# Kernel optimization log

Measured on AMD Instinct MI355X. Metric: run time of the kernel, lower is better.

The kernel has to match this reference:

```python
import math
import jax, jax.numpy as jnp
import numpy as np

EMBED, HEADS, LEVELS, POINTS = 256, 8, 4, 4
HEAD_DIM = EMBED // HEADS
SHAPES = ((100, 100), (50, 50), (25, 25), (13, 13))  # (h, w) per level
BS, NQ = 8, 900
NV = sum(h * w for h, w in SHAPES)


def _offset_bias():
    # Faithful to init_weights(): per-head rotated grid init for sampling_offsets bias.
    th = np.arange(HEADS, dtype=np.float32) * (2.0 * math.pi / HEADS)
    g = np.stack([np.cos(th), np.sin(th)], -1)
    g = g / np.abs(g).max(-1, keepdims=True)
    g = np.tile(g[:, None, None, :], (1, LEVELS, POINTS, 1))
    g = g * (np.arange(POINTS, dtype=np.float32) + 1.0)[None, None, :, None]
    return jnp.asarray(g.reshape(-1))


def setup_inputs() -> dict:
    key = jax.random.key(0)
    ks = jax.random.split(key, 10)
    s = 0.05
    return {
        "query": jax.random.normal(ks[0], (BS, NQ, EMBED), jnp.float32),
        "value": jax.random.normal(ks[1], (BS, NV, EMBED), jnp.float32),
        "reference_points": jax.random.uniform(ks[2], (BS, NQ, LEVELS, 2), jnp.float32),
        "spatial_shapes": jnp.array(SHAPES, jnp.int32),
        "W_off": jax.random.normal(ks[3], (EMBED, HEADS * LEVELS * POINTS * 2), jnp.float32) * s,
        "b_off": _offset_bias(),
        "W_attn": jax.random.normal(ks[4], (EMBED, HEADS * LEVELS * POINTS), jnp.float32) * s,
        "b_attn": jnp.zeros((HEADS * LEVELS * POINTS,), jnp.float32),
        "W_v": jax.random.normal(ks[5], (EMBED, EMBED), jnp.float32) * s,
        "b_v": jnp.zeros((EMBED,), jnp.float32),
        "W_out": jax.random.normal(ks[6], (EMBED, EMBED), jnp.float32) * s,
        "b_out": jnp.zeros((EMBED,), jnp.float32),
    }


def _bilinear_sample(vl, loc, H, W, aw):
    """grid_sample bilinear, align_corners=False, zero padding, fused with attn weights.

    vl:  (bs, heads, H*W, d)   loc: (bs, nq, heads, P, 2) in [0,1] (x, y)
    aw:  (bs, heads, nq, P)    ->   (bs, heads, nq, d)
    """
    x = loc[..., 0] * W - 0.5
    y = loc[..., 1] * H - 0.5
    x0 = jnp.floor(x)
    y0 = jnp.floor(y)
    lx = x - x0
    ly = y - y0
    x0i = x0.astype(jnp.int32)
    y0i = y0.astype(jnp.int32)
    bs, heads = vl.shape[0], vl.shape[1]
    nq, P = loc.shape[1], loc.shape[3]
    acc = jnp.zeros((bs, heads, nq, vl.shape[-1]), vl.dtype)
    corners = ((0, 0, (1 - lx) * (1 - ly)), (1, 0, lx * (1 - ly)),
               (0, 1, (1 - lx) * ly), (1, 1, lx * ly))
    for dx, dy, wgt in corners:
        xi = x0i + dx
        yi = y0i + dy
        valid = ((xi >= 0) & (xi < W) & (yi >= 0) & (yi < H)).astype(vl.dtype)
        idx = jnp.clip(yi, 0, H - 1) * W + jnp.clip(xi, 0, W - 1)  # (bs, nq, heads, P)
        idx = idx.transpose(0, 2, 1, 3).reshape(bs, heads, nq * P)
        g = jnp.take_along_axis(vl, idx[..., None], axis=2).reshape(bs, heads, nq, P, -1)
        cw = (wgt * valid).transpose(0, 2, 1, 3) * aw  # (bs, heads, nq, P)
        acc = acc + (g * cw[..., None]).sum(3)
    return acc


def reference(query, value, reference_points, spatial_shapes,
              W_off, b_off, W_attn, b_attn, W_v, b_v, W_out, b_out):
    identity = query
    bs, nq, _ = query.shape
    v = (value @ W_v + b_v).reshape(bs, -1, HEADS, HEAD_DIM)
    off = (query @ W_off + b_off).reshape(bs, nq, HEADS, LEVELS, POINTS, 2)
    aw = (query @ W_attn + b_attn).reshape(bs, nq, HEADS, LEVELS * POINTS)
    aw = jax.nn.softmax(aw, -1).reshape(bs, nq, HEADS, LEVELS, POINTS)
    # offset normalizer is (w, h) per level
    norm = jnp.stack([spatial_shapes[:, 1], spatial_shapes[:, 0]], -1).astype(query.dtype)
    loc = reference_points[:, :, None, :, None, :] + off / norm[None, None, None, :, None, :]
    sizes = [h * w for h, w in SHAPES]
    starts = np.cumsum([0] + sizes[:-1])
    out = jnp.zeros((bs, HEADS, nq, HEAD_DIM), query.dtype)
    for l, (h, w) in enumerate(SHAPES):
        vl = jax.lax.dynamic_slice_in_dim(v, int(starts[l]), sizes[l], axis=1)
        vl = vl.transpose(0, 2, 1, 3)  # (bs, heads, h*w, d)
        aw_l = aw[:, :, :, l].transpose(0, 2, 1, 3)  # (bs, heads, nq, P)
        out = out + _bilinear_sample(vl, loc[:, :, :, l], h, w, aw_l)
    out = out.transpose(0, 2, 1, 3).reshape(bs, nq, EMBED)
    return out @ W_out + b_out + identity
```

## Files before the change

kernel.cpp:

```cpp
#include <hip/hip_runtime.h>
#include <hip/hip_bf16.h>

#define EMBED    256
#define HEADS    8
#define LEVELS   4
#define POINTS   4
#define HEAD_DIM 32
#define BS       8
#define NQ       900
#define NV       13294
#define MV       (BS*NV)
#define MQ       (BS*NQ)
#define NQOUT    384

typedef float  f32x4  __attribute__((ext_vector_type(4)));
typedef __bf16 bf16x8 __attribute__((ext_vector_type(8)));
typedef unsigned short ushort8  __attribute__((ext_vector_type(8)));
typedef unsigned short ushort4v __attribute__((ext_vector_type(4)));

__device__ __forceinline__ unsigned short f2bf(float f) {
    unsigned u = __builtin_bit_cast(unsigned, f);
    u += 0x7FFFu + ((u >> 16) & 1u);
    return (unsigned short)(u >> 16);
}
__device__ __forceinline__ float bf2f(unsigned short h) {
    unsigned u = ((unsigned)h) << 16;
    return __builtin_bit_cast(float, u);
}

__global__ __launch_bounds__(256) void prep_kernel(
    const float* __restrict__ Wv,  const float* __restrict__ Woff,
    const float* __restrict__ Wattn, const float* __restrict__ Wout,
    const float* __restrict__ boff, const float* __restrict__ battn,
    unsigned short* __restrict__ WtV, unsigned short* __restrict__ WtQ,
    unsigned short* __restrict__ WtO, float* __restrict__ biasQ)
{
    int n = blockIdx.x;
    int k = threadIdx.x;
    if (n < 256) {
        WtV[n * 256 + k] = f2bf(Wv [k * 256 + n]);
        WtO[n * 256 + k] = f2bf(Wout[k * 256 + n]);
        WtQ[n * 256 + k] = f2bf(Woff[k * 256 + n]);
    } else {
        int j = n - 256;
        WtQ[n * 256 + k] = f2bf(Wattn[k * 128 + j]);
    }
    if (k == 0) biasQ[n] = (n < 256) ? boff[n] : battn[n - 256];
}

#define WLDK 264

template <int COLSETS, int PAR, bool OUT_BF16, bool ADD_ID>
__global__ __launch_bounds__(COLSETS * PAR * 64)
void gemm_ldsw(const float* __restrict__ A,
               const unsigned short* __restrict__ Bt,
               const float* __restrict__ bias,
               const float* __restrict__ Ident,
               void* __restrict__ Cv, int M, int Ntot)
{
    constexpr int NC   = COLSETS * 64;
    constexpr int NTHR = COLSETS * PAR * 64;
    const int n0g = blockIdx.y * NC;
    __shared__ unsigned short Ws[NC * WLDK];

    const int tid = threadIdx.x;
    #pragma unroll
    for (int i = 0; i < (NC * 32) / NTHR; ++i) {
        int flat = i * NTHR + tid;
        int row = flat >> 5, col = (flat & 31) * 8;
        *(ushort8*)&Ws[row * WLDK + col] =
            *(const ushort8*)(Bt + (size_t)(n0g + row) * 256 + col);
    }
    __syncthreads();

    const int wave = tid >> 6, lane = tid & 63;
    const int colset = wave % COLSETS, parity = wave / COLSETS;
    const int lrow = lane & 15, kq = lane >> 4;
    const int n0 = colset * 64;

    f32x4 bj[4];
    #pragma unroll
    for (int j = 0; j < 4; ++j)
        bj[j] = *(const f32x4*)(bias + n0g + n0 + j * 16 + kq * 4);

    const int NS    = M / 16;
    const int chunk = (NS + gridDim.x - 1) / gridDim.x;
    const int send  = min(NS, blockIdx.x * chunk + chunk);
    int s = blockIdx.x * chunk + parity;
    if (s >= send) return;

    auto loadHalf = [&](f32x4 (&b)[8], int ss, int h) {
        const float* ab = A + (size_t)(ss * 16 + lrow) * 256 + h * 128 + kq * 8;
        #pragma unroll
        for (int c = 0; c < 4; ++c) {
            b[2 * c]     = *(const f32x4*)(ab + c * 32);
            b[2 * c + 1] = *(const f32x4*)(ab + c * 32 + 4);
        }
    };
    auto computeHalf = [&](f32x4 (&b)[8], int h, f32x4 (&acc)[4]) {
        #pragma unroll
        for (int c = 0; c < 4; ++c) {
            ushort8 vb;
            #pragma unroll
            for (int e = 0; e < 4; ++e) {
                vb[e]     = f2bf(b[2 * c][e]);
                vb[4 + e] = f2bf(b[2 * c + 1][e]);
            }
            bf16x8 vf = __builtin_bit_cast(bf16x8, vb);
            #pragma unroll
            for (int j = 0; j < 4; ++j) {
                bf16x8 wf = *(const bf16x8*)
                    &Ws[(n0 + j * 16 + lrow) * WLDK + h * 128 + c * 32 + kq * 8];
                acc[j] = __builtin_amdgcn_mfma_f32_16x16x32_bf16(wf, vf, acc[j], 0, 0, 0);
            }
        }
    };

    f32x4 b0[8], b1[8];
    loadHalf(b0, s, 0);
    while (true) {
        loadHalf(b1, s, 1);
        f32x4 acc[4];
        #pragma unroll
        for (int j = 0; j < 4; ++j) acc[j] = (f32x4)0.f;
        computeHalf(b0, 0, acc);
        const int sn = s + PAR;
        const bool more = sn < send;
        if (more) loadHalf(b0, sn, 0);
        computeHalf(b1, 1, acc);

        const size_t crow = (size_t)(s * 16 + lrow) * Ntot + n0g + n0 + kq * 4;
        #pragma unroll
        for (int j = 0; j < 4; ++j) {
            f32x4 r = acc[j] + bj[j];
            if (ADD_ID)
                r += *(const f32x4*)(Ident + crow + j * 16);
            if (OUT_BF16) {
                ushort4v o;
                #pragma unroll
                for (int e = 0; e < 4; ++e) o[e] = f2bf(r[e]);
                *(ushort4v*)((unsigned short*)Cv + crow + j * 16) = o;
            } else {
                *(f32x4*)((float*)Cv + crow + j * 16) = r;
            }
        }
        if (!more) break;
        s = sn;
    }
}

__device__ const int   LVL_W[4]  = {100, 50, 25, 13};
__device__ const int   LVL_H[4]  = {100, 50, 25, 13};
__device__ const int   LVL_S[4]  = {0, 10000, 12500, 13125};

__global__ __launch_bounds__(256) void sample_kernel(
    const unsigned short* __restrict__ V,
    const float* __restrict__ Qout,
    const float* __restrict__ RP,
    float* __restrict__ OutS)
{
    const int gid = blockIdx.x * 16 + (threadIdx.x >> 4);
    const int s   = threadIdx.x & 15;
    const int h   = gid & 7;
    const int bq  = gid >> 3;
    const int b   = bq / NQ;

    const float* qrow = Qout + (size_t)bq * NQOUT;

    const int l = s >> 2;
    const float ox = qrow[h * 32 + 2 * s];
    const float oy = qrow[h * 32 + 2 * s + 1];
    float logit    = qrow[256 + h * 16 + s];
    const float rpx = RP[((size_t)bq * 4 + l) * 2 + 0];
    const float rpy = RP[((size_t)bq * 4 + l) * 2 + 1];
    const int W = LVL_W[l], H = LVL_H[l], st = LVL_S[l];
    float x = rpx * (float)W + ox - 0.5f;
    float y = rpy * (float)H + oy - 0.5f;
    float fx = floorf(x), fy = floorf(y);
    float lx = x - fx, ly = y - fy;
    int x0 = (int)fx, y0 = (int)fy;
    int x1 = x0 + 1,  y1 = y0 + 1;

    float mx = logit;
    #pragma unroll
    for (int o = 8; o; o >>= 1) mx = fmaxf(mx, __shfl_xor(mx, o, 16));
    float e = __expf(logit - mx);
    float sum = e;
    #pragma unroll
    for (int o = 8; o; o >>= 1) sum += __shfl_xor(sum, o, 16);
    const float wgt = e / sum;

    const float vx0 = (x0 >= 0 && x0 < W) ? 1.f : 0.f;
    const float vx1 = (x1 >= 0 && x1 < W) ? 1.f : 0.f;
    const float vy0 = (y0 >= 0 && y0 < H) ? 1.f : 0.f;
    const float vy1 = (y1 >= 0 && y1 < H) ? 1.f : 0.f;
    const int cx0 = min(max(x0, 0), W - 1), cx1 = min(max(x1, 0), W - 1);
    const int cy0 = min(max(y0, 0), H - 1), cy1 = min(max(y1, 0), H - 1);
    float w00 = wgt * (1.f - lx) * (1.f - ly) * vx0 * vy0;
    float w10 = wgt * lx * (1.f - ly) * vx1 * vy0;
    float w01 = wgt * (1.f - lx) * ly * vx0 * vy1;
    float w11 = wgt * lx * ly * vx1 * vy1;
    int i00 = st + cy0 * W + cx0;
    int i10 = st + cy0 * W + cx1;
    int i01 = st + cy1 * W + cx0;
    int i11 = st + cy1 * W + cx1;

    const unsigned short* vb = V + ((size_t)b * NV) * 256 + h * 32 + 2 * s;
    float ax0 = 0.f, ay0 = 0.f, ax1 = 0.f, ay1 = 0.f;

    #pragma unroll
    for (int sp = 0; sp < 16; ++sp) {
        int   j00 = __shfl(i00, sp, 16), j10 = __shfl(i10, sp, 16);
        int   j01 = __shfl(i01, sp, 16), j11 = __shfl(i11, sp, 16);
        float u00 = __shfl(w00, sp, 16), u10 = __shfl(w10, sp, 16);
        float u01 = __shfl(w01, sp, 16), u11 = __shfl(w11, sp, 16);
        unsigned p00 = *(const unsigned*)(vb + (size_t)j00 * 256);
        unsigned p10 = *(const unsigned*)(vb + (size_t)j10 * 256);
        unsigned p01 = *(const unsigned*)(vb + (size_t)j01 * 256);
        unsigned p11 = *(const unsigned*)(vb + (size_t)j11 * 256);
        ax0 = fmaf(u00, bf2f((unsigned short)(p00 & 0xFFFF)), ax0);
        ay0 = fmaf(u00, bf2f((unsigned short)(p00 >> 16)), ay0);
        ax1 = fmaf(u10, bf2f((unsigned short)(p10 & 0xFFFF)), ax1);
        ay1 = fmaf(u10, bf2f((unsigned short)(p10 >> 16)), ay1);
        ax0 = fmaf(u01, bf2f((unsigned short)(p01 & 0xFFFF)), ax0);
        ay0 = fmaf(u01, bf2f((unsigned short)(p01 >> 16)), ay0);
        ax1 = fmaf(u11, bf2f((unsigned short)(p11 & 0xFFFF)), ax1);
        ay1 = fmaf(u11, bf2f((unsigned short)(p11 >> 16)), ay1);
    }
    float2* o = (float2*)(OutS + (size_t)bq * 256 + h * 32);
    o[s] = make_float2(ax0 + ax1, ay0 + ay1);
}

extern "C" void kernel_launch(void* const* d_in, const int* in_sizes, int n_in,
                              void* d_out, int out_size, void* d_ws, size_t ws_size,
                              hipStream_t stream)
{
    const float* query  = (const float*)d_in[0];
    const float* value  = (const float*)d_in[1];
    const float* rp     = (const float*)d_in[2];
    const float* W_off  = (const float*)d_in[4];
    const float* b_off  = (const float*)d_in[5];
    const float* W_attn = (const float*)d_in[6];
    const float* b_attn = (const float*)d_in[7];
    const float* W_v    = (const float*)d_in[8];
    const float* b_v    = (const float*)d_in[9];
    const float* W_out  = (const float*)d_in[10];
    const float* b_out  = (const float*)d_in[11];

    char* ws = (char*)d_ws;
    size_t off = 0;
    unsigned short* Vbf = (unsigned short*)(ws + off); off += (size_t)MV * 256 * 2;
    float* qout         = (float*)(ws + off);          off += (size_t)MQ * NQOUT * 4;
    float* outs         = (float*)(ws + off);          off += (size_t)MQ * 256 * 4;
    unsigned short* WtV = (unsigned short*)(ws + off); off += 256 * 256 * 2;
    unsigned short* WtQ = (unsigned short*)(ws + off); off += 384 * 256 * 2;
    unsigned short* WtO = (unsigned short*)(ws + off); off += 256 * 256 * 2;
    float* biasQ        = (float*)(ws + off);          off += 384 * 4;

    prep_kernel<<<384, 256, 0, stream>>>(W_v, W_off, W_attn, W_out, b_off, b_attn,
                                         WtV, WtQ, WtO, biasQ);

    gemm_ldsw<2, 4, true, false><<<dim3(256, 2), 512, 0, stream>>>(
        value, WtV, b_v, nullptr, Vbf, MV, 256);

    gemm_ldsw<2, 4, false, false><<<dim3(57, 3), 512, 0, stream>>>(
        query, WtQ, biasQ, nullptr, qout, MQ, NQOUT);

    sample_kernel<<<(BS * NQ * HEADS) / 16, 256, 0, stream>>>(Vbf, qout, rp, outs);

    gemm_ldsw<2, 4, false, true><<<dim3(57, 2), 512, 0, stream>>>(
        outs, WtO, b_out, query, (float*)d_out, MQ, 256);
}
```

Baseline: 273.4 us.

## Add dedicated value-projection GEMM holding the full weight in swizzled LDS

Replaces the generic two-column-set value projection GEMM with a specialized kernel. Each 1024-thread block loads the entire 256x256 bf16 weight into XOR-swizzled shared memory once and has each wave compute full 16-row x 256-column output strips. The activations are therefore read once instead of once per column block. This uses 128KB of LDS and many accumulator registers per lane, which limits occupancy to one block per CU.

```diff
diff --git a/kernel.cpp b/kernel.cpp
--- a/kernel.cpp
+++ b/kernel.cpp
@@ -46,6 +46,79 @@
         WtQ[n * 256 + k] = f2bf(Wattn[k * 128 + j]);
     }
     if (k == 0) biasQ[n] = (n < 256) ? boff[n] : battn[n - 256];
+}
+
+__global__ __launch_bounds__(1024)
+void gemm_v(const float* __restrict__ A,
+            const unsigned short* __restrict__ Bt,
+            const float* __restrict__ bias,
+            unsigned short* __restrict__ C)
+{
+    __shared__ unsigned short Ws[256 * 256];
+    __shared__ float Bs[256];
+
+    const int tid = threadIdx.x;
+    #pragma unroll
+    for (int i = 0; i < 8; ++i) {
+        int flat = i * 1024 + tid;
+        int row = flat >> 5, col16 = flat & 31;
+        int swz = (col16 ^ (row & 7)) * 8;
+        *(ushort8*)&Ws[row * 256 + swz] =
+            *(const ushort8*)(Bt + (size_t)row * 256 + col16 * 8);
+    }
+    if (tid < 256) Bs[tid] = bias[tid];
+    __syncthreads();
+
+    const int wave = tid >> 6, lane = tid & 63;
+    const int lrow = lane & 15, kq = lane >> 4;
+    const int rswz = (lrow & 7) << 3;
+
+    const int NS    = MV / 16;
+    const int chunk = (NS + gridDim.x - 1) / gridDim.x;
+    const int base  = blockIdx.x * chunk;
+    const int send  = min(NS, base + chunk);
+
+    for (int s = base + wave; s < send; s += 16) {
+        const float* ab = A + (size_t)(s * 16 + lrow) * 256 + kq * 8;
+        f32x4 tv[16];
+        #pragma unroll
+        for (int c = 0; c < 8; ++c) {
+            tv[2 * c]     = *(const f32x4*)(ab + c * 32);
+            tv[2 * c + 1] = *(const f32x4*)(ab + c * 32 + 4);
+        }
+        bf16x8 av[8];
+        #pragma unroll
+        for (int c = 0; c < 8; ++c) {
+            ushort8 vb;
+            #pragma unroll
+            for (int e = 0; e < 4; ++e) {
+                vb[e]     = f2bf(tv[2 * c][e]);
+                vb[4 + e] = f2bf(tv[2 * c + 1][e]);
+            }
+            av[c] = __builtin_bit_cast(bf16x8, vb);
+        }
+        f32x4 acc[16];
+        #pragma unroll
+        for (int j = 0; j < 16; ++j) acc[j] = (f32x4)0.f;
+        #pragma unroll
+        for (int c = 0; c < 8; ++c) {
+            const int wcol = (c * 32 + kq * 8) ^ rswz;
+            #pragma unroll
+            for (int j = 0; j < 16; ++j) {
+                bf16x8 wf = *(const bf16x8*)&Ws[(j * 16 + lrow) * 256 + wcol];
+                acc[j] = __builtin_amdgcn_mfma_f32_16x16x32_bf16(wf, av[c], acc[j], 0, 0, 0);
+            }
+        }
+        const size_t crow = (size_t)(s * 16 + lrow) * 256 + kq * 4;
+        #pragma unroll
+        for (int j = 0; j < 16; ++j) {
+            f32x4 r = acc[j] + *(const f32x4*)&Bs[j * 16 + kq * 4];
+            ushort4v o;
+            #pragma unroll
+            for (int e = 0; e < 4; ++e) o[e] = f2bf(r[e]);
+            *(ushort4v*)(C + crow + j * 16) = o;
+        }
+    }
 }
 
 #define WLDK 264
@@ -260,8 +333,7 @@
     prep_kernel<<<384, 256, 0, stream>>>(W_v, W_off, W_attn, W_out, b_off, b_attn,
                                          WtV, WtQ, WtO, biasQ);
 
-    gemm_ldsw<2, 4, true, false><<<dim3(256, 2), 512, 0, stream>>>(
-        value, WtV, b_v, nullptr, Vbf, MV, 256);
+    gemm_v<<<256, 1024, 0, stream>>>(value, WtV, b_v, Vbf);
 
     gemm_ldsw<2, 4, false, false><<<dim3(57, 3), 512, 0, stream>>>(
         query, WtQ, biasQ, nullptr, qout, MQ, NQOUT);
```

After: 603.2 us. 2.21x slower.
